# Performance work log

Measured on AMD Instinct MI355X. Metric: run time of the kernel, lower is better.

The kernel has to match this reference:

```python
import jax, jax.numpy as jnp
import numpy as np


def _ste(q, x):
    # straight-through estimator: forward = q, gradient = identity w.r.t. x
    return x + jax.lax.stop_gradient(q - x)


def quant_w(w, bit_w=8):
    # symmetric per-tensor weight quantization fused into QConv2d
    qmax = 2.0 ** (bit_w - 1) - 1.0
    scale = jnp.max(jnp.abs(w)) / qmax
    q = jnp.clip(jnp.round(w / scale), -qmax, qmax) * scale
    return _ste(q, w)


def quant_a(x, bit_a=8):
    # unsigned activation quantizer: clamp to [0,1], uniform bit_a levels
    n = 2.0 ** bit_a - 1.0
    xc = jnp.clip(x, 0.0, 1.0)
    q = jnp.round(xc * n) / n
    return _ste(q, xc)


def exp_norm2d(x, gamma, beta, eps=1e-5):
    # instance-style norm: per (N, C) statistics over spatial dims, affine
    mean = jnp.mean(x, axis=(2, 3), keepdims=True)
    var = jnp.var(x, axis=(2, 3), keepdims=True)
    xn = (x - mean) * jax.lax.rsqrt(var + eps)
    return xn * gamma[None, :, None, None] + beta[None, :, None, None]


def qconv(x, w, stride, pad, bit_w=8):
    wq = quant_w(w, bit_w)
    return jax.lax.conv_general_dilated(
        x, wq, window_strides=(stride, stride),
        padding=[(pad, pad), (pad, pad)],
        dimension_numbers=('NCHW', 'OIHW', 'NCHW'))


def setup_inputs() -> dict:
    key = jax.random.key(0)
    ks = jax.random.split(key, 4)
    C_in, C_out, H = 256, 512, 56
    return {
        'x': jax.random.normal(ks[0], (32, C_in, H, H), jnp.float32),
        'w1': jax.random.normal(ks[1], (C_out, C_in, 3, 3), jnp.float32) * 0.05,
        'g1': jnp.ones((C_out,), jnp.float32),
        'b1': jnp.zeros((C_out,), jnp.float32),
        'w2': jax.random.normal(ks[2], (C_out, C_out, 3, 3), jnp.float32) * 0.05,
        'g2': jnp.ones((C_out,), jnp.float32),
        'b2': jnp.zeros((C_out,), jnp.float32),
        'wp': jax.random.normal(ks[3], (C_out, C_in, 1, 1), jnp.float32) * 0.05,
        'gp': jnp.ones((C_out,), jnp.float32),
        'bp': jnp.zeros((C_out,), jnp.float32),
    }


def reference(x, w1, g1, b1, w2, g2, b2, wp, gp, bp):
    # main branch: QConv(s2) -> ExpNorm -> act quant -> QConv(s1) -> ExpNorm
    h = qconv(x, w1, stride=2, pad=1)
    h = exp_norm2d(h, g1, b1)
    h = quant_a(h, bit_a=8)
    h = qconv(h, w2, stride=1, pad=1)
    h = exp_norm2d(h, g2, b2)
    # projection shortcut: QConv 1x1 stride 2 -> ExpNorm
    s = qconv(x, wp, stride=2, pad=0)
    s = exp_norm2d(s, gp, bp)
    return h + s
```

## Files before the change

kernel.cpp:

```cpp
#include <hip/hip_runtime.h>
#include <cstdint>
#include <cstddef>


typedef unsigned short ushort_t;
typedef __attribute__((ext_vector_type(8))) short bf16x8;
typedef __attribute__((ext_vector_type(4))) float f32x4;
typedef __attribute__((ext_vector_type(4))) int i32x4;

#define NB   32
#define C_IN 256
#define HIN  56
#define CO   512
#define OHW  784
#define OWD  28
#define MTOT (NB * OHW)

constexpr size_t OFF_XH   = 0;
constexpr size_t OFF_A1   = OFF_XH  + 51380224;
constexpr size_t OFF_H2   = OFF_A1  + 25690112;
constexpr size_t OFF_S    = OFF_H2  + 51380224;
constexpr size_t OFF_WT1  = OFF_S   + 51380224;
constexpr size_t OFF_WT2  = OFF_WT1 + 2359296;
constexpr size_t OFF_WTP  = OFF_WT2 + 4718592;
constexpr size_t OFF_PSUM = OFF_WTP + 262144;
constexpr size_t OFF_A1N  = OFF_PSUM + 2097152;
constexpr size_t OFF_B1N  = OFF_A1N + 65536;
constexpr size_t OFF_A2N  = OFF_B1N + 65536;
constexpr size_t OFF_B2N  = OFF_A2N + 65536;
constexpr size_t OFF_APN  = OFF_B2N + 65536;
constexpr size_t OFF_BPN  = OFF_APN + 65536;
constexpr size_t OFF_MX   = OFF_BPN + 65536;
constexpr size_t OFF_ZB   = OFF_MX  + 16;
constexpr size_t OFF_CS   = OFF_ZB  + 2048;

__device__ __forceinline__ ushort_t f2bf(float f) {
    unsigned u = __float_as_uint(f);
    u += 0x7FFFu + ((u >> 16) & 1u);
    return (ushort_t)(u >> 16);
}
__device__ __forceinline__ float bf2f(ushort_t u) {
    return __uint_as_float(((unsigned)u) << 16);
}

__device__ __forceinline__ void async_copy16(const void* g, const void* l) {
    auto gp = (const __attribute__((address_space(1))) unsigned int*)(uintptr_t)g;
    auto lp = (__attribute__((address_space(3))) unsigned int*)(unsigned int)(uintptr_t)l;
    __builtin_amdgcn_global_load_lds(gp, lp, 16, 0, 0);
}

__global__ void to_nhwc_k(const float* __restrict__ x, ushort_t* __restrict__ xh) {
    __shared__ float tile[64][33];
    const int wt0 = blockIdx.x * 32;
    const int ct0 = blockIdx.y * 64;
    const int nh  = blockIdx.z;
    const int n = nh / HIN, h = nh - n * HIN;
    {
        const int tx = threadIdx.x & 31;
        const int ty = threadIdx.x >> 5;
        const int w  = wt0 + tx;
#pragma unroll
        for (int j = 0; j < 8; ++j) {
            int cl = ty + j * 8;
            if (w < HIN)
                tile[cl][tx] = x[(((size_t)n * C_IN + ct0 + cl) * HIN + h) * HIN + w];
        }
    }
    __syncthreads();
    {
        const int tc = threadIdx.x & 63;
        const int tw = threadIdx.x >> 6;
#pragma unroll
        for (int j = 0; j < 8; ++j) {
            int wl = tw + j * 4;
            int w  = wt0 + wl;
            if (w < HIN)
                xh[(((size_t)n * HIN + h) * HIN + w) * C_IN + ct0 + tc] =
                    f2bf(tile[tc][wl]);
        }
    }
}

__global__ void absmax3_k(const float* __restrict__ w1, int n1,
                          const float* __restrict__ w2, int n2,
                          const float* __restrict__ wp, int np,
                          unsigned* out) {
    const float* w; int nelem;
    if (blockIdx.y == 0)      { w = w1; nelem = n1; }
    else if (blockIdx.y == 1) { w = w2; nelem = n2; }
    else                      { w = wp; nelem = np; }
    int stride = gridDim.x * blockDim.x;
    float m = 0.f;
    for (int i = blockIdx.x * blockDim.x + threadIdx.x; i < nelem; i += stride)
        m = fmaxf(m, fabsf(w[i]));
#pragma unroll
    for (int off = 32; off > 0; off >>= 1)
        m = fmaxf(m, __shfl_down(m, off));
    if ((threadIdx.x & 63) == 0) atomicMax(out + blockIdx.y, __float_as_uint(m));
}

template <int CO_, int CI_, int KHW_>
__global__ void quantw_k(const float* __restrict__ w, const unsigned* __restrict__ mx,
                         ushort_t* __restrict__ wt) {
    const int total = KHW_ * CO_ * CI_;
    int idx = blockIdx.x * 256 + threadIdx.x;
    if (idx >= total) return;
    float scale = __uint_as_float(*mx) * (1.0f / 127.0f);
    float inv   = scale > 0.f ? 1.0f / scale : 0.f;
    int khw = idx / (CO_ * CI_);
    int r   = idx - khw * (CO_ * CI_);
    int co  = r / CI_;
    int ci  = r - co * CI_;
    float v  = w[((size_t)co * CI_ + ci) * KHW_ + khw];
    float qv = rintf(v * inv);
    qv = fminf(127.f, fmaxf(-127.f, qv));
    wt[idx] = f2bf(qv * scale);
}

__global__ void quantw_i8_k(const float* __restrict__ w, const unsigned* __restrict__ mx,
                            signed char* __restrict__ wt) {
    const int total = 9 * CO * CO;
    int idx = blockIdx.x * 256 + threadIdx.x;
    if (idx >= total) return;
    float scale = __uint_as_float(*mx) * (1.0f / 127.0f);
    float inv   = scale > 0.f ? 1.0f / scale : 0.f;
    int khw = idx / (CO * CO);
    int r   = idx - khw * (CO * CO);
    int co  = r / CO;
    int ci  = r - co * CO;
    float v  = w[((size_t)co * CO + ci) * 9 + khw];
    float qv = rintf(v * inv);
    qv = fminf(127.f, fmaxf(-127.f, qv));
    wt[idx] = (signed char)(int)qv;
}

__global__ void colsum_k(const signed char* __restrict__ wt, float* __restrict__ cs) {
    const int khw = blockIdx.x;
    const int co  = blockIdx.y * 32 + (threadIdx.x & 31);
    const int cig = threadIdx.x >> 5;
    const signed char* p = wt + ((size_t)khw * CO + co) * CO + cig * 64;
    int s = 0;
#pragma unroll
    for (int i = 0; i < 64; ++i) s += p[i];
    __shared__ int red[8][32];
    red[cig][threadIdx.x & 31] = s;
    __syncthreads();
    if (cig == 0) {
        int tot = 0;
#pragma unroll
        for (int g = 0; g < 8; ++g) tot += red[g][threadIdx.x & 31];
        cs[khw * CO + co] = (float)tot;
    }
}

template <int CIN, int KH, int KW, int STRIDE, int PAD, int IH, int IW>
__launch_bounds__(512, 2)
__global__ void conv8p_k(const ushort_t* __restrict__ xin,
                         const ushort_t* __restrict__ wt,
                         ushort_t* __restrict__ out,
                         const ushort_t* __restrict__ zbuf,
                         float* __restrict__ psum, float* __restrict__ pss) {
    constexpr int BK  = 64;
    constexpr int CKT = CIN / BK;
    constexpr int KT  = KH * KW * CKT;

    __shared__ alignas(16) short As[2 * 256 * BK];
    __shared__ alignas(16) short Bs[2 * 256 * BK];

    const int tid  = threadIdx.x;
    const int lane = tid & 63;
    const int wv   = tid >> 6;
    const int wm   = wv >> 2;
    const int wn   = wv & 3;
    const int lrow = lane & 15;
    const int lq   = lane >> 4;
    const int sw   = lrow & 7;

    const int bid = blockIdx.x;
    const int xcd = bid & 7;
    const int j   = bid >> 3;
    const int wg  = (xcd < 4 ? xcd * 25 : 100 + (xcd - 4) * 24) + j;
    const int m0  = (wg >> 1) * 256;
    const int co0 = (wg & 1) * 256;

    const int arow = tid >> 3;
    const int ach  = tid & 7;
    long abase[4]; unsigned amask[4]; int bco[4];
#pragma unroll
    for (int c = 0; c < 4; ++c) {
        int row = c * 64 + arow;
        int m   = m0 + row;
        int n   = m / OHW;
        int sp  = m - n * OHW;
        int oh  = sp / OWD, ow = sp - oh * OWD;
        int ihb = oh * STRIDE - PAD, iwb = ow * STRIDE - PAD;
        int swz = (ach ^ (row & 7)) * 8;
        abase[c] = ((long)n * (IH * IW) + (long)ihb * IW + iwb) * CIN + swz;
        unsigned mk = 0;
#pragma unroll
        for (int kh = 0; kh < KH; ++kh)
#pragma unroll
            for (int kw = 0; kw < KW; ++kw) {
                int ih = ihb + kh, iw = iwb + kw;
                if ((unsigned)ih < (unsigned)IH && (unsigned)iw < (unsigned)IW)
                    mk |= 1u << (kh * KW + kw);
            }
        amask[c] = mk;
        bco[c]   = (co0 + row) * CIN + swz;
    }

    auto stageA = [&](int c, int nb, long aoff, int khw) {
        const ushort_t* src = ((amask[c] >> khw) & 1)
            ? xin + (abase[c] + aoff) : zbuf;
        async_copy16(src, (const void*)&As[nb * 16384 + c * 4096 + wv * 512]);
    };
    auto stageB = [&](int c, int nb, int boff) {
        async_copy16(wt + (boff + bco[c]),
                     (const void*)&Bs[nb * 16384 + c * 4096 + wv * 512]);
    };

    f32x4 acc[8][4];
#pragma unroll
    for (int a = 0; a < 8; ++a)
#pragma unroll
        for (int b = 0; b < 4; ++b) acc[a][b] = {0.f, 0.f, 0.f, 0.f};

    stageB(0, 0, 0); stageB(1, 0, 0); stageB(2, 0, 0); stageB(3, 0, 0);
    stageA(0, 0, 0, 0); stageA(1, 0, 0, 0); stageA(2, 0, 0, 0); stageA(3, 0, 0, 0);
    asm volatile("s_waitcnt vmcnt(0)" ::: "memory");
    __builtin_amdgcn_s_barrier();

    int  khw_n = 0, kw_n = 0, ck_n = 1;
    long aoff_n = BK;
    int  boff_n = BK;

    int cur = 0;
    for (int t = 0; t < KT; ++t) {
        const bool hn = (t + 1 < KT);
        const int  nb = cur ^ 1;
        const short* Acur = &As[cur * 16384];
        const short* Bcur = &Bs[cur * 16384];

        if (hn) {
            stageB(0, nb, boff_n); stageB(1, nb, boff_n);
            stageB(2, nb, boff_n); stageB(3, nb, boff_n);
            stageA(0, nb, aoff_n, khw_n); stageA(1, nb, aoff_n, khw_n);
            stageA(2, nb, aoff_n, khw_n); stageA(3, nb, aoff_n, khw_n);
        }
        __builtin_amdgcn_sched_barrier(0);

        bf16x8 af[4][2], bfr[2][2][2];

#pragma unroll
        for (int mi = 0; mi < 4; ++mi) {
            const int row = wm * 128 + mi * 16 + lrow;
#pragma unroll
            for (int ks = 0; ks < 2; ++ks) {
                const int ch = ((ks * 4 + lq) ^ sw) * 8;
                af[mi][ks] = *(const bf16x8*)&Acur[row * BK + ch];
            }
        }
#pragma unroll
        for (int qn = 0; qn < 2; ++qn)
#pragma unroll
            for (int ni = 0; ni < 2; ++ni) {
                const int row = wn * 64 + qn * 32 + ni * 16 + lrow;
#pragma unroll
                for (int ks = 0; ks < 2; ++ks) {
                    const int ch = ((ks * 4 + lq) ^ sw) * 8;
                    bfr[qn][ni][ks] = *(const bf16x8*)&Bcur[row * BK + ch];
                }
            }
#pragma unroll
        for (int mi = 0; mi < 4; ++mi)
#pragma unroll
            for (int qn = 0; qn < 2; ++qn)
#pragma unroll
                for (int ni = 0; ni < 2; ++ni)
#pragma unroll
                    for (int ks = 0; ks < 2; ++ks)
                        acc[mi][qn * 2 + ni] =
                            __builtin_amdgcn_mfma_f32_16x16x32_bf16(
                                af[mi][ks], bfr[qn][ni][ks],
                                acc[mi][qn * 2 + ni], 0, 0, 0);

#pragma unroll
        for (int mi = 0; mi < 4; ++mi) {
            const int row = wm * 128 + 64 + mi * 16 + lrow;
#pragma unroll
            for (int ks = 0; ks < 2; ++ks) {
                const int ch = ((ks * 4 + lq) ^ sw) * 8;
                af[mi][ks] = *(const bf16x8*)&Acur[row * BK + ch];
            }
        }
#pragma unroll
        for (int mi = 0; mi < 4; ++mi)
#pragma unroll
            for (int qn = 0; qn < 2; ++qn)
#pragma unroll
                for (int ni = 0; ni < 2; ++ni)
#pragma unroll
                    for (int ks = 0; ks < 2; ++ks)
                        acc[4 + mi][qn * 2 + ni] =
                            __builtin_amdgcn_mfma_f32_16x16x32_bf16(
                                af[mi][ks], bfr[qn][ni][ks],
                                acc[4 + mi][qn * 2 + ni], 0, 0, 0);

        asm volatile("s_waitcnt vmcnt(0)" ::: "memory");
        __builtin_amdgcn_sched_barrier(0);
        __builtin_amdgcn_s_barrier();

        if (hn) {
            ck_n++;
            if (ck_n == CKT) {
                ck_n = 0; khw_n++; kw_n++;
                if (kw_n == KW) { kw_n = 0; aoff_n += (long)(IW - KW) * CIN + BK; }
                else            { aoff_n += BK; }
                boff_n += (CO - 1) * CIN + BK;
            } else {
                aoff_n += BK; boff_n += BK;
            }
        }
        cur ^= 1;
    }

    const int mb = m0 + wm * 128 + lq * 4;
    const int cb = co0 + wn * 64 + lrow;
#pragma unroll
    for (int mi = 0; mi < 8; ++mi)
#pragma unroll
        for (int ni = 0; ni < 4; ++ni)
#pragma unroll
            for (int r = 0; r < 4; ++r)
                out[(size_t)(mb + mi * 16 + r) * CO + (cb + ni * 16)] =
                    f2bf(acc[mi][ni][r]);

    const int n0 = m0 / OHW;
    const int mS = (n0 + 1) * OHW;
    float sv[2][4], qv[2][4];
#pragma unroll
    for (int g = 0; g < 2; ++g)
#pragma unroll
        for (int ni = 0; ni < 4; ++ni) { sv[g][ni] = 0.f; qv[g][ni] = 0.f; }
#pragma unroll
    for (int mi = 0; mi < 8; ++mi)
#pragma unroll
        for (int ni = 0; ni < 4; ++ni)
#pragma unroll
            for (int r = 0; r < 4; ++r) {
                float v = acc[mi][ni][r];
                int m = mb + mi * 16 + r;
                int g = (m >= mS) ? 1 : 0;
                sv[g][ni] += v; qv[g][ni] += v * v;
            }
#pragma unroll
    for (int d = 16; d <= 32; d <<= 1)
#pragma unroll
        for (int g = 0; g < 2; ++g)
#pragma unroll
            for (int ni = 0; ni < 4; ++ni) {
                sv[g][ni] += __shfl_xor(sv[g][ni], d);
                qv[g][ni] += __shfl_xor(qv[g][ni], d);
            }
    if (lq == 0) {
        const bool split = (mS < m0 + 256);
#pragma unroll
        for (int ni = 0; ni < 4; ++ni) {
            atomicAdd(&psum[n0 * CO + cb + ni * 16], sv[0][ni]);
            atomicAdd(&pss [n0 * CO + cb + ni * 16], qv[0][ni]);
            if (split) {
                atomicAdd(&psum[(n0 + 1) * CO + cb + ni * 16], sv[1][ni]);
                atomicAdd(&pss [(n0 + 1) * CO + cb + ni * 16], qv[1][ni]);
            }
        }
    }
}

__launch_bounds__(512, 2)
__global__ void conv_i8_k(const signed char* __restrict__ xin,
                          const signed char* __restrict__ wt,
                          const float* __restrict__ colsum,
                          const unsigned* __restrict__ mxp,
                          ushort_t* __restrict__ out,
                          const signed char* __restrict__ zbuf,
                          float* __restrict__ psum, float* __restrict__ pss) {
    constexpr int CIN = 512, BK = 64, CKT = 8, KT = 72;
    constexpr int IH = 28, IW = 28;

    __shared__ alignas(16) signed char As[2 * 256 * BK];
    __shared__ alignas(16) signed char Bs[2 * 256 * BK];

    const int tid  = threadIdx.x;
    const int lane = tid & 63;
    const int wv   = tid >> 6;
    const int wm   = wv >> 2;
    const int wn   = wv & 3;
    const int lrow = lane & 15;
    const int lq   = lane >> 4;

    const int bid = blockIdx.x;
    const int xcd = bid & 7;
    const int j   = bid >> 3;
    const int wg  = (xcd < 4 ? xcd * 25 : 100 + (xcd - 4) * 24) + j;
    const int m0  = (wg >> 1) * 256;
    const int co0 = (wg & 1) * 256;

    const int arow2 = tid >> 2;
    const int ach2  = tid & 3;
    long abase[2]; unsigned amask[2]; int bco[2];
#pragma unroll
    for (int c = 0; c < 2; ++c) {
        int row = c * 128 + arow2;
        int m   = m0 + row;
        int n   = m / OHW;
        int sp  = m - n * OHW;
        int oh  = sp / OWD, ow = sp - oh * OWD;
        int ihb = oh - 1, iwb = ow - 1;
        int swz = (ach2 ^ (row & 3)) * 16;
        abase[c] = ((long)n * (IH * IW) + (long)ihb * IW + iwb) * CIN + swz;
        unsigned mk = 0;
#pragma unroll
        for (int kh = 0; kh < 3; ++kh)
#pragma unroll
            for (int kw = 0; kw < 3; ++kw) {
                int ih = ihb + kh, iw = iwb + kw;
                if ((unsigned)ih < (unsigned)IH && (unsigned)iw < (unsigned)IW)
                    mk |= 1u << (kh * 3 + kw);
            }
        amask[c] = mk;
        bco[c]   = (co0 + row) * CIN + swz;
    }

    auto stageA = [&](int c, int nb, long aoff, int khw) {
        const signed char* src = ((amask[c] >> khw) & 1)
            ? xin + (abase[c] + aoff) : zbuf;
        async_copy16(src, (const void*)&As[nb * 16384 + c * 8192 + wv * 1024]);
    };
    auto stageB = [&](int c, int nb, int boff) {
        async_copy16(wt + (boff + bco[c]),
                     (const void*)&Bs[nb * 16384 + c * 8192 + wv * 1024]);
    };

    i32x4 acc[8][4];
#pragma unroll
    for (int a = 0; a < 8; ++a)
#pragma unroll
        for (int b = 0; b < 4; ++b) acc[a][b] = {0, 0, 0, 0};

    stageB(0, 0, 0); stageB(1, 0, 0);
    stageA(0, 0, 0, 0); stageA(1, 0, 0, 0);
    asm volatile("s_waitcnt vmcnt(0)" ::: "memory");
    __builtin_amdgcn_s_barrier();

    int  khw_n = 0, kw_n = 0, ck_n = 1;
    long aoff_n = BK;
    int  boff_n = BK;

    int cur = 0;
    for (int t = 0; t < KT; ++t) {
        const bool hn = (t + 1 < KT);
        const int  nb = cur ^ 1;
        const signed char* Acur = &As[cur * 16384];
        const signed char* Bcur = &Bs[cur * 16384];

        if (hn) {
            stageB(0, nb, boff_n); stageB(1, nb, boff_n);
            stageA(0, nb, aoff_n, khw_n); stageA(1, nb, aoff_n, khw_n);
        }
        __builtin_amdgcn_sched_barrier(0);

        i32x4 af[8], bfr[4];
#pragma unroll
        for (int mi = 0; mi < 8; ++mi) {
            const int row = wm * 128 + mi * 16 + lrow;
            const int byt = row * BK + ((lq ^ (row & 3)) * 16);
            af[mi] = *(const i32x4*)&Acur[byt];
        }
#pragma unroll
        for (int ni = 0; ni < 4; ++ni) {
            const int row = wn * 64 + ni * 16 + lrow;
            const int byt = row * BK + ((lq ^ (row & 3)) * 16);
            bfr[ni] = *(const i32x4*)&Bcur[byt];
        }
#pragma unroll
        for (int mi = 0; mi < 8; ++mi)
#pragma unroll
            for (int ni = 0; ni < 4; ++ni)
                acc[mi][ni] = __builtin_amdgcn_mfma_i32_16x16x64_i8(
                    af[mi], bfr[ni], acc[mi][ni], 0, 0, 0);

        asm volatile("s_waitcnt vmcnt(0)" ::: "memory");
        __builtin_amdgcn_sched_barrier(0);
        __builtin_amdgcn_s_barrier();

        if (hn) {
            ck_n++;
            if (ck_n == CKT) {
                ck_n = 0; khw_n++; kw_n++;
                if (kw_n == 3) { kw_n = 0; aoff_n += (long)(IW - 3) * CIN + BK; }
                else           { aoff_n += BK; }
                boff_n += (CO - 1) * CIN + BK;
            } else {
                aoff_n += BK; boff_n += BK;
            }
        }
        cur ^= 1;
    }

    const int mb = m0 + wm * 128 + lq * 4;
    const int cb = co0 + wn * 64 + lrow;
    const float scale = __uint_as_float(*mxp) * (1.0f / 127.0f);
    const float sc    = scale * (1.0f / 255.0f);
    const float c128  = 128.0f * sc;

    float Sall[4], Sr0[4], Sr2[4], Sc0[4], Sc2[4], K0[4], K2[4], K6[4], K8[4];
#pragma unroll
    for (int ni = 0; ni < 4; ++ni) {
        float cs[9];
#pragma unroll
        for (int k = 0; k < 9; ++k) cs[k] = colsum[k * CO + cb + ni * 16];
        Sall[ni] = cs[0]+cs[1]+cs[2]+cs[3]+cs[4]+cs[5]+cs[6]+cs[7]+cs[8];
        Sr0[ni] = cs[0]+cs[1]+cs[2];  Sr2[ni] = cs[6]+cs[7]+cs[8];
        Sc0[ni] = cs[0]+cs[3]+cs[6];  Sc2[ni] = cs[2]+cs[5]+cs[8];
        K0[ni] = cs[0]; K2[ni] = cs[2]; K6[ni] = cs[6]; K8[ni] = cs[8];
    }

    const int n0 = m0 / OHW;
    const int mS = (n0 + 1) * OHW;
    float sv[2][4], qvv[2][4];
#pragma unroll
    for (int g = 0; g < 2; ++g)
#pragma unroll
        for (int ni = 0; ni < 4; ++ni) { sv[g][ni] = 0.f; qvv[g][ni] = 0.f; }

#pragma unroll
    for (int mi = 0; mi < 8; ++mi)
#pragma unroll
        for (int r = 0; r < 4; ++r) {
            const int m  = mb + mi * 16 + r;
            const int n  = m / OHW;
            const int sp = m - n * OHW;
            const int oh = sp / OWD, ow = sp - oh * OWD;
            const int g  = (m >= mS) ? 1 : 0;
#pragma unroll
            for (int ni = 0; ni < 4; ++ni) {
                float T = Sall[ni];
                if (oh == 0)       T -= Sr0[ni];
                if (oh == OWD - 1) T -= Sr2[ni];
                if (ow == 0)       T -= Sc0[ni];
                if (ow == OWD - 1) T -= Sc2[ni];
                if (oh == 0 && ow == 0)             T += K0[ni];
                if (oh == 0 && ow == OWD - 1)       T += K2[ni];
                if (oh == OWD - 1 && ow == 0)       T += K6[ni];
                if (oh == OWD - 1 && ow == OWD - 1) T += K8[ni];
                float val = sc * (float)acc[mi][ni][r] + c128 * T;
                out[(size_t)m * CO + (cb + ni * 16)] = f2bf(val);
                sv[g][ni] += val; qvv[g][ni] += val * val;
            }
        }
#pragma unroll
    for (int d = 16; d <= 32; d <<= 1)
#pragma unroll
        for (int g = 0; g < 2; ++g)
#pragma unroll
            for (int ni = 0; ni < 4; ++ni) {
                sv[g][ni]  += __shfl_xor(sv[g][ni], d);
                qvv[g][ni] += __shfl_xor(qvv[g][ni], d);
            }
    if (lq == 0) {
        const bool split = (mS < m0 + 256);
#pragma unroll
        for (int ni = 0; ni < 4; ++ni) {
            atomicAdd(&psum[n0 * CO + cb + ni * 16], sv[0][ni]);
            atomicAdd(&pss [n0 * CO + cb + ni * 16], qvv[0][ni]);
            if (split) {
                atomicAdd(&psum[(n0 + 1) * CO + cb + ni * 16], sv[1][ni]);
                atomicAdd(&pss [(n0 + 1) * CO + cb + ni * 16], qvv[1][ni]);
            }
        }
    }
}

__global__ void statsf3_k(const float* __restrict__ ps0, const float* __restrict__ qs0,
                          const float* __restrict__ g0, const float* __restrict__ bb0,
                          float* __restrict__ ao0, float* __restrict__ bo0,
                          const float* __restrict__ ps1, const float* __restrict__ qs1,
                          const float* __restrict__ g1, const float* __restrict__ bb1,
                          float* __restrict__ ao1, float* __restrict__ bo1,
                          const float* __restrict__ ps2, const float* __restrict__ qs2,
                          const float* __restrict__ g2, const float* __restrict__ bb2,
                          float* __restrict__ ao2, float* __restrict__ bo2) {
    const float *ps, *qs, *g, *bb; float *ao, *bo;
    if (blockIdx.y == 0)      { ps = ps0; qs = qs0; g = g0; bb = bb0; ao = ao0; bo = bo0; }
    else if (blockIdx.y == 1) { ps = ps1; qs = qs1; g = g1; bb = bb1; ao = ao1; bo = bo1; }
    else                      { ps = ps2; qs = qs2; g = g2; bb = bb2; ao = ao2; bo = bo2; }
    int idx = blockIdx.x * 256 + threadIdx.x;
    int c = idx & 511;
    float s  = ps[idx];
    float ss = qs[idx];
    float mean = s * (1.0f / 784.0f);
    float var  = ss * (1.0f / 784.0f) - mean * mean;
    float rstd = rsqrtf(var + 1e-5f);
    float a = rstd * g[c];
    ao[idx] = a;
    bo[idx] = bb[c] - mean * a;
}

__global__ void norm_quant_i8_k(const ushort_t* __restrict__ h, const float* __restrict__ a_,
                                const float* __restrict__ b_, signed char* __restrict__ o) {
    int idx = blockIdx.x * 256 + threadIdx.x;
    int row = idx >> 6;
    int c0  = (idx & 63) * 8;
    int n   = row / OHW;
    bf16x8 v = ((const bf16x8*)h)[idx];
    const float* ap = a_ + n * CO + c0;
    const float* bp = b_ + n * CO + c0;
    unsigned lo = 0, hi = 0;
#pragma unroll
    for (int k = 0; k < 8; ++k) {
        float f = bf2f((ushort_t)v[k]) * ap[k] + bp[k];
        float kq = rintf(fminf(fmaxf(f, 0.f), 1.f) * 255.f);
        int s8 = (int)kq - 128;
        unsigned b = (unsigned)(s8 & 0xFF);
        if (k < 4) lo |= b << (8 * k);
        else       hi |= b << (8 * (k - 4));
    }
    ((uint2*)o)[idx] = make_uint2(lo, hi);
}

__global__ void final_k(const ushort_t* __restrict__ h2, const ushort_t* __restrict__ s,
                        const float* __restrict__ a2, const float* __restrict__ b2,
                        const float* __restrict__ ap_, const float* __restrict__ bp_,
                        float* __restrict__ out) {
    __shared__ float tile[64][33];
    const int sp0 = blockIdx.x * 32;
    const int c0  = blockIdx.y * 64;
    const int n   = blockIdx.z;
    const int tx  = threadIdx.x & 31;
    const int ty  = threadIdx.x >> 5;
#pragma unroll
    for (int j = 0; j < 4; ++j) {
        int spl = ty + j * 8;
        int sp  = sp0 + spl;
        if (sp < OHW) {
            int c = c0 + tx * 2;
            size_t ix = ((size_t)n * OHW + sp) * CO + c;
            int ci = n * CO + c;
            ushort2 vh = *(const ushort2*)&h2[ix];
            ushort2 vs = *(const ushort2*)&s[ix];
            tile[tx * 2][spl] =
                bf2f(vh.x) * a2[ci] + b2[ci] + bf2f(vs.x) * ap_[ci] + bp_[ci];
            tile[tx * 2 + 1][spl] =
                bf2f(vh.y) * a2[ci + 1] + b2[ci + 1] + bf2f(vs.y) * ap_[ci + 1] + bp_[ci + 1];
        }
    }
    __syncthreads();
    const int sp = sp0 + tx;
#pragma unroll
    for (int j = 0; j < 8; ++j) {
        int cl = ty + j * 8;
        if (sp < OHW)
            out[((size_t)n * CO + c0 + cl) * OHW + sp] = tile[cl][tx];
    }
}

extern "C" void kernel_launch(void* const* d_in, const int* in_sizes, int n_in,
                              void* d_out, int out_size, void* d_ws, size_t ws_size,
                              hipStream_t stream) {
    const float* x  = (const float*)d_in[0];
    const float* w1 = (const float*)d_in[1];
    const float* g1 = (const float*)d_in[2];
    const float* b1 = (const float*)d_in[3];
    const float* w2 = (const float*)d_in[4];
    const float* g2 = (const float*)d_in[5];
    const float* b2 = (const float*)d_in[6];
    const float* wp = (const float*)d_in[7];
    const float* gp = (const float*)d_in[8];
    const float* bp = (const float*)d_in[9];
    float* out = (float*)d_out;
    char* ws = (char*)d_ws;

    ushort_t*    xh    = (ushort_t*)(ws + OFF_XH);
    signed char* a1    = (signed char*)(ws + OFF_A1);
    ushort_t*    h2    = (ushort_t*)(ws + OFF_H2);
    ushort_t*    sbuf  = (ushort_t*)(ws + OFF_S);
    ushort_t*    wt1   = (ushort_t*)(ws + OFF_WT1);
    signed char* wt2i  = (signed char*)(ws + OFF_WT2);
    ushort_t*    wtp   = (ushort_t*)(ws + OFF_WTP);
    float*    psum1 = (float*)(ws + OFF_PSUM);
    float*    pss1  = (float*)(ws + OFF_PSUM + 65536);
    float*    psum2 = (float*)(ws + OFF_PSUM + 131072);
    float*    pss2  = (float*)(ws + OFF_PSUM + 196608);
    float*    psump = (float*)(ws + OFF_PSUM + 262144);
    float*    pssp  = (float*)(ws + OFF_PSUM + 327680);
    float*    a1n  = (float*)(ws + OFF_A1N);
    float*    b1n  = (float*)(ws + OFF_B1N);
    float*    a2n  = (float*)(ws + OFF_A2N);
    float*    b2n  = (float*)(ws + OFF_B2N);
    float*    apn  = (float*)(ws + OFF_APN);
    float*    bpn  = (float*)(ws + OFF_BPN);
    unsigned* mx   = (unsigned*)(ws + OFF_MX);
    ushort_t* zb   = (ushort_t*)(ws + OFF_ZB);
    float*    cs   = (float*)(ws + OFF_CS);
    ushort_t* h1   = (ushort_t*)out;

    hipMemsetAsync(ws + OFF_MX, 0, 16 + 2048, stream);
    hipMemsetAsync(ws + OFF_PSUM, 0, 393216, stream);

    to_nhwc_k<<<dim3(2, 4, NB * HIN), 256, 0, stream>>>(x, xh);
    absmax3_k<<<dim3(512, 3), 256, 0, stream>>>(w1, CO * C_IN * 9,
                                                w2, CO * CO * 9,
                                                wp, C_IN * CO, mx);
    quantw_k<CO, C_IN, 9><<<dim3(4608), 256, 0, stream>>>(w1, mx + 0, wt1);
    quantw_i8_k<<<dim3(9216), 256, 0, stream>>>(w2, mx + 1, wt2i);
    quantw_k<CO, C_IN, 1><<<dim3(512), 256, 0, stream>>>(wp, mx + 2, wtp);
    colsum_k<<<dim3(9, 16), 256, 0, stream>>>(wt2i, cs);

    conv8p_k<C_IN, 3, 3, 2, 1, HIN, HIN>
        <<<dim3(196), 512, 0, stream>>>(xh, wt1, h1, (const ushort_t*)zb, psum1, pss1);
    statsf3_k<<<dim3(64, 1), 256, 0, stream>>>(psum1, pss1, g1, b1, a1n, b1n,
                                               psum1, pss1, g1, b1, a1n, b1n,
                                               psum1, pss1, g1, b1, a1n, b1n);
    norm_quant_i8_k<<<dim3(MTOT * CO / 8 / 256), 256, 0, stream>>>(h1, a1n, b1n, a1);

    conv_i8_k<<<dim3(196), 512, 0, stream>>>(a1, wt2i, cs, mx + 1, h2,
                                             (const signed char*)zb, psum2, pss2);
    conv8p_k<C_IN, 1, 1, 2, 0, HIN, HIN>
        <<<dim3(196), 512, 0, stream>>>(xh, wtp, sbuf, (const ushort_t*)zb, psump, pssp);

    statsf3_k<<<dim3(64, 2), 256, 0, stream>>>(psum2, pss2, g2, b2, a2n, b2n,
                                               psump, pssp, gp, bp, apn, bpn,
                                               psum2, pss2, g2, b2, a2n, b2n);

    final_k<<<dim3(25, 8, NB), 256, 0, stream>>>(h2, sbuf, a2n, b2n, apn, bpn, out);
}
```

Before: 319.5 us.

## Shrink int8 conv tile to 128x128 and launch four times more blocks

Reworks the int8 3x3 conv from 256x256 output tiles over 196 blocks to 128x128 tiles over 784 blocks. LDS use drops to a quarter, launch bounds now allow 4 blocks per CU, the LDS swizzle pattern changes, the XCD-aware block remap is simplified and offsets move to 32-bit. The aim is better occupancy and more latency hiding on a GPU whose 196 blocks did not fill it. In exchange each tile gets less operand reuse, so more global and LDS traffic is needed per MFMA and there are more atomic stat updates.

```diff
diff --git a/kernel.cpp b/kernel.cpp
--- a/kernel.cpp
+++ b/kernel.cpp
@@ -376,7 +376,7 @@
     }
 }
 
-__launch_bounds__(512, 2)
+__launch_bounds__(512, 4)
 __global__ void conv_i8_k(const signed char* __restrict__ xin,
                           const signed char* __restrict__ wt,
                           const float* __restrict__ colsum,
@@ -387,8 +387,8 @@
     constexpr int CIN = 512, BK = 64, CKT = 8, KT = 72;
     constexpr int IH = 28, IW = 28;
 
-    __shared__ alignas(16) signed char As[2 * 256 * BK];
-    __shared__ alignas(16) signed char Bs[2 * 256 * BK];
+    __shared__ alignas(16) signed char As[2 * 128 * BK];
+    __shared__ alignas(16) signed char Bs[2 * 128 * BK];
 
     const int tid  = threadIdx.x;
     const int lane = tid & 63;
@@ -399,25 +399,22 @@
     const int lq   = lane >> 4;
 
     const int bid = blockIdx.x;
-    const int xcd = bid & 7;
-    const int j   = bid >> 3;
-    const int wg  = (xcd < 4 ? xcd * 25 : 100 + (xcd - 4) * 24) + j;
-    const int m0  = (wg >> 1) * 256;
-    const int co0 = (wg & 1) * 256;
-
-    const int arow2 = tid >> 2;
-    const int ach2  = tid & 3;
-    long abase[2]; unsigned amask[2]; int bco[2];
-#pragma unroll
-    for (int c = 0; c < 2; ++c) {
-        int row = c * 128 + arow2;
-        int m   = m0 + row;
+    const int wg  = (bid & 7) * 98 + (bid >> 3);
+    const int m0  = (wg >> 2) * 128;
+    const int co0 = (wg & 3) * 128;
+
+    const int arow = tid >> 2;
+    const int ach  = tid & 3;
+    const int fsw  = (arow >> 1) & 3;
+    int abase; unsigned amask; int bco;
+    {
+        int m   = m0 + arow;
         int n   = m / OHW;
         int sp  = m - n * OHW;
         int oh  = sp / OWD, ow = sp - oh * OWD;
         int ihb = oh - 1, iwb = ow - 1;
-        int swz = (ach2 ^ (row & 3)) * 16;
-        abase[c] = ((long)n * (IH * IW) + (long)ihb * IW + iwb) * CIN + swz;
+        int swz = (ach ^ fsw) * 16;
+        abase = (n * (IH * IW) + ihb * IW + iwb) * CIN + swz;
         unsigned mk = 0;
 #pragma unroll
         for (int kh = 0; kh < 3; ++kh)
@@ -427,65 +424,60 @@
                 if ((unsigned)ih < (unsigned)IH && (unsigned)iw < (unsigned)IW)
                     mk |= 1u << (kh * 3 + kw);
             }
-        amask[c] = mk;
-        bco[c]   = (co0 + row) * CIN + swz;
-    }
-
-    auto stageA = [&](int c, int nb, long aoff, int khw) {
-        const signed char* src = ((amask[c] >> khw) & 1)
-            ? xin + (abase[c] + aoff) : zbuf;
-        async_copy16(src, (const void*)&As[nb * 16384 + c * 8192 + wv * 1024]);
+        amask = mk;
+        bco = (co0 + arow) * CIN + swz;
+    }
+
+    auto stageA = [&](int nb, int aoff, int khw) {
+        const signed char* src = ((amask >> khw) & 1)
+            ? xin + (abase + aoff) : zbuf;
+        async_copy16(src, (const void*)&As[nb * 8192 + wv * 1024]);
     };
-    auto stageB = [&](int c, int nb, int boff) {
-        async_copy16(wt + (boff + bco[c]),
-                     (const void*)&Bs[nb * 16384 + c * 8192 + wv * 1024]);
+    auto stageB = [&](int nb, int boff) {
+        async_copy16(wt + (boff + bco),
+                     (const void*)&Bs[nb * 8192 + wv * 1024]);
     };
 
-    i32x4 acc[8][4];
-#pragma unroll
-    for (int a = 0; a < 8; ++a)
-#pragma unroll
-        for (int b = 0; b < 4; ++b) acc[a][b] = {0, 0, 0, 0};
-
-    stageB(0, 0, 0); stageB(1, 0, 0);
-    stageA(0, 0, 0, 0); stageA(1, 0, 0, 0);
+    i32x4 acc[4][2];
+#pragma unroll
+    for (int a = 0; a < 4; ++a)
+#pragma unroll
+        for (int b = 0; b < 2; ++b) acc[a][b] = {0, 0, 0, 0};
+
+    stageB(0, 0);
+    stageA(0, 0, 0);
     asm volatile("s_waitcnt vmcnt(0)" ::: "memory");
     __builtin_amdgcn_s_barrier();
 
-    int  khw_n = 0, kw_n = 0, ck_n = 1;
-    long aoff_n = BK;
-    int  boff_n = BK;
+    int khw_n = 0, kw_n = 0, ck_n = 1;
+    int aoff_n = BK;
+    int boff_n = BK;
 
     int cur = 0;
     for (int t = 0; t < KT; ++t) {
         const bool hn = (t + 1 < KT);
         const int  nb = cur ^ 1;
-        const signed char* Acur = &As[cur * 16384];
-        const signed char* Bcur = &Bs[cur * 16384];
-
-        if (hn) {
-            stageB(0, nb, boff_n); stageB(1, nb, boff_n);
-            stageA(0, nb, aoff_n, khw_n); stageA(1, nb, aoff_n, khw_n);
-        }
+        const signed char* Acur = &As[cur * 8192];
+        const signed char* Bcur = &Bs[cur * 8192];
+
+        if (hn) { stageB(nb, boff_n); stageA(nb, aoff_n, khw_n); }
         __builtin_amdgcn_sched_barrier(0);
 
-        i32x4 af[8], bfr[4];
-#pragma unroll
-        for (int mi = 0; mi < 8; ++mi) {
-            const int row = wm * 128 + mi * 16 + lrow;
-            const int byt = row * BK + ((lq ^ (row & 3)) * 16);
-            af[mi] = *(const i32x4*)&Acur[byt];
-        }
-#pragma unroll
-        for (int ni = 0; ni < 4; ++ni) {
-            const int row = wn * 64 + ni * 16 + lrow;
-            const int byt = row * BK + ((lq ^ (row & 3)) * 16);
-            bfr[ni] = *(const i32x4*)&Bcur[byt];
-        }
-#pragma unroll
-        for (int mi = 0; mi < 8; ++mi)
-#pragma unroll
-            for (int ni = 0; ni < 4; ++ni)
+        i32x4 af[4], bfr[2];
+#pragma unroll
+        for (int mi = 0; mi < 4; ++mi) {
+            const int row = wm * 64 + mi * 16 + lrow;
+            af[mi] = *(const i32x4*)&Acur[row * BK + ((lq ^ ((row >> 1) & 3)) * 16)];
+        }
+#pragma unroll
+        for (int ni = 0; ni < 2; ++ni) {
+            const int row = wn * 32 + ni * 16 + lrow;
+            bfr[ni] = *(const i32x4*)&Bcur[row * BK + ((lq ^ ((row >> 1) & 3)) * 16)];
+        }
+#pragma unroll
+        for (int mi = 0; mi < 4; ++mi)
+#pragma unroll
+            for (int ni = 0; ni < 2; ++ni)
                 acc[mi][ni] = __builtin_amdgcn_mfma_i32_16x16x64_i8(
                     af[mi], bfr[ni], acc[mi][ni], 0, 0, 0);
 
@@ -497,7 +489,7 @@
             ck_n++;
             if (ck_n == CKT) {
                 ck_n = 0; khw_n++; kw_n++;
-                if (kw_n == 3) { kw_n = 0; aoff_n += (long)(IW - 3) * CIN + BK; }
+                if (kw_n == 3) { kw_n = 0; aoff_n += (IW - 3) * CIN + BK; }
                 else           { aoff_n += BK; }
                 boff_n += (CO - 1) * CIN + BK;
             } else {
@@ -507,15 +499,15 @@
         cur ^= 1;
     }
 
-    const int mb = m0 + wm * 128 + lq * 4;
-    const int cb = co0 + wn * 64 + lrow;
+    const int mb = m0 + wm * 64 + lq * 4;
+    const int cb = co0 + wn * 32 + lrow;
     const float scale = __uint_as_float(*mxp) * (1.0f / 127.0f);
     const float sc    = scale * (1.0f / 255.0f);
     const float c128  = 128.0f * sc;
 
-    float Sall[4], Sr0[4], Sr2[4], Sc0[4], Sc2[4], K0[4], K2[4], K6[4], K8[4];
-#pragma unroll
-    for (int ni = 0; ni < 4; ++ni) {
+    float Sall[2], Sr0[2], Sr2[2], Sc0[2], Sc2[2], K0[2], K2[2], K6[2], K8[2];
+#pragma unroll
+    for (int ni = 0; ni < 2; ++ni) {
         float cs[9];
 #pragma unroll
         for (int k = 0; k < 9; ++k) cs[k] = colsum[k * CO + cb + ni * 16];
@@ -527,14 +519,14 @@
 
     const int n0 = m0 / OHW;
     const int mS = (n0 + 1) * OHW;
-    float sv[2][4], qvv[2][4];
+    float sv[2][2], qvv[2][2];
 #pragma unroll
     for (int g = 0; g < 2; ++g)
 #pragma unroll
-        for (int ni = 0; ni < 4; ++ni) { sv[g][ni] = 0.f; qvv[g][ni] = 0.f; }
-
-#pragma unroll
-    for (int mi = 0; mi < 8; ++mi)
+        for (int ni = 0; ni < 2; ++ni) { sv[g][ni] = 0.f; qvv[g][ni] = 0.f; }
+
+#pragma unroll
+    for (int mi = 0; mi < 4; ++mi)
 #pragma unroll
         for (int r = 0; r < 4; ++r) {
             const int m  = mb + mi * 16 + r;
@@ -543,7 +535,7 @@
             const int oh = sp / OWD, ow = sp - oh * OWD;
             const int g  = (m >= mS) ? 1 : 0;
 #pragma unroll
-            for (int ni = 0; ni < 4; ++ni) {
+            for (int ni = 0; ni < 2; ++ni) {
                 float T = Sall[ni];
                 if (oh == 0)       T -= Sr0[ni];
                 if (oh == OWD - 1) T -= Sr2[ni];
@@ -563,14 +555,14 @@
 #pragma unroll
         for (int g = 0; g < 2; ++g)
 #pragma unroll
-            for (int ni = 0; ni < 4; ++ni) {
+            for (int ni = 0; ni < 2; ++ni) {
                 sv[g][ni]  += __shfl_xor(sv[g][ni], d);
                 qvv[g][ni] += __shfl_xor(qvv[g][ni], d);
             }
     if (lq == 0) {
-        const bool split = (mS < m0 + 256);
-#pragma unroll
-        for (int ni = 0; ni < 4; ++ni) {
+        const bool split = (mS < m0 + 128);
+#pragma unroll
+        for (int ni = 0; ni < 2; ++ni) {
             atomicAdd(&psum[n0 * CO + cb + ni * 16], sv[0][ni]);
             atomicAdd(&pss [n0 * CO + cb + ni * 16], qvv[0][ni]);
             if (split) {
@@ -723,7 +715,7 @@
                                                psum1, pss1, g1, b1, a1n, b1n);
     norm_quant_i8_k<<<dim3(MTOT * CO / 8 / 256), 256, 0, stream>>>(h1, a1n, b1n, a1);
 
-    conv_i8_k<<<dim3(196), 512, 0, stream>>>(a1, wt2i, cs, mx + 1, h2,
+    conv_i8_k<<<dim3(784), 512, 0, stream>>>(a1, wt2i, cs, mx + 1, h2,
                                              (const signed char*)zb, psum2, pss2);
     conv8p_k<C_IN, 1, 1, 2, 0, HIN, HIN>
         <<<dim3(196), 512, 0, stream>>>(xh, wtp, sbuf, (const ushort_t*)zb, psump, pssp);
```

After: 342.5 us. 7.2% more time.

## Merge 3x3 and 1x1 strided convs into one launch; change int8 LDS swizzle

Applied to the files above, without the earlier changes.

The stride-2 3x3 conv and the 1x1 projection conv, both reading the NHWC input, now run as one kernel with 392 blocks. Each block picks its conv type from its block index, with the two types interleaved across XCDs. This is meant to fill the GPU with more concurrent work and let the cheap 1x1 tiles fill the tail of the 3x3 grid. In exchange the conv shape becomes runtime values, so loop unrolling and constant folding are lost. The int8 conv's LDS XOR swizzle also changes from row&3 to (row>>1)&3 to reduce bank conflicts.

```diff
diff --git a/kernel.cpp b/kernel.cpp
--- a/kernel.cpp
+++ b/kernel.cpp
@@ -153,16 +153,17 @@
     }
 }
 
-template <int CIN, int KH, int KW, int STRIDE, int PAD, int IH, int IW>
 __launch_bounds__(512, 2)
-__global__ void conv8p_k(const ushort_t* __restrict__ xin,
-                         const ushort_t* __restrict__ wt,
-                         ushort_t* __restrict__ out,
-                         const ushort_t* __restrict__ zbuf,
-                         float* __restrict__ psum, float* __restrict__ pss) {
-    constexpr int BK  = 64;
-    constexpr int CKT = CIN / BK;
-    constexpr int KT  = KH * KW * CKT;
+__global__ void convmix_k(const ushort_t* __restrict__ xin,
+                          const ushort_t* __restrict__ wt1,
+                          const ushort_t* __restrict__ wtp,
+                          ushort_t* __restrict__ out1,
+                          ushort_t* __restrict__ outp,
+                          const ushort_t* __restrict__ zbuf,
+                          float* __restrict__ psum1, float* __restrict__ pss1,
+                          float* __restrict__ psump, float* __restrict__ pssp) {
+    constexpr int CIN = 256, BK = 64, CKT = 4;
+    constexpr int IH = HIN, IW = HIN;
 
     __shared__ alignas(16) short As[2 * 256 * BK];
     __shared__ alignas(16) short Bs[2 * 256 * BK];
@@ -176,12 +177,21 @@
     const int lq   = lane >> 4;
     const int sw   = lrow & 7;
 
-    const int bid = blockIdx.x;
-    const int xcd = bid & 7;
-    const int j   = bid >> 3;
-    const int wg  = (xcd < 4 ? xcd * 25 : 100 + (xcd - 4) * 24) + j;
-    const int m0  = (wg >> 1) * 256;
-    const int co0 = (wg & 1) * 256;
+    const int bid  = blockIdx.x;
+    const int wg   = (bid & 7) * 49 + (bid >> 3);
+    const int type = wg & 1;
+    const int tl   = wg >> 1;
+    const int m0   = (tl >> 1) * 256;
+    const int co0  = (tl & 1) * 256;
+
+    const int KH  = type ? 1 : 3;
+    const int KW  = KH;
+    const int PAD = type ? 0 : 1;
+    const int KT  = KH * KW * CKT;
+    const ushort_t* wt  = type ? wtp : wt1;
+    ushort_t*       out = type ? outp : out1;
+    float* psum = type ? psump : psum1;
+    float* pss  = type ? pssp  : pss1;
 
     const int arow = tid >> 3;
     const int ach  = tid & 7;
@@ -193,13 +203,11 @@
         int n   = m / OHW;
         int sp  = m - n * OHW;
         int oh  = sp / OWD, ow = sp - oh * OWD;
-        int ihb = oh * STRIDE - PAD, iwb = ow * STRIDE - PAD;
+        int ihb = oh * 2 - PAD, iwb = ow * 2 - PAD;
         int swz = (ach ^ (row & 7)) * 8;
         abase[c] = ((long)n * (IH * IW) + (long)ihb * IW + iwb) * CIN + swz;
         unsigned mk = 0;
-#pragma unroll
         for (int kh = 0; kh < KH; ++kh)
-#pragma unroll
             for (int kw = 0; kw < KW; ++kw) {
                 int ih = ihb + kh, iw = iwb + kw;
                 if ((unsigned)ih < (unsigned)IH && (unsigned)iw < (unsigned)IW)
@@ -416,7 +424,7 @@
         int sp  = m - n * OHW;
         int oh  = sp / OWD, ow = sp - oh * OWD;
         int ihb = oh - 1, iwb = ow - 1;
-        int swz = (ach2 ^ (row & 3)) * 16;
+        int swz = (ach2 ^ ((row >> 1) & 3)) * 16;
         abase[c] = ((long)n * (IH * IW) + (long)ihb * IW + iwb) * CIN + swz;
         unsigned mk = 0;
 #pragma unroll
@@ -473,14 +481,12 @@
 #pragma unroll
         for (int mi = 0; mi < 8; ++mi) {
             const int row = wm * 128 + mi * 16 + lrow;
-            const int byt = row * BK + ((lq ^ (row & 3)) * 16);
-            af[mi] = *(const i32x4*)&Acur[byt];
+            af[mi] = *(const i32x4*)&Acur[row * BK + ((lq ^ ((row >> 1) & 3)) * 16)];
         }
 #pragma unroll
         for (int ni = 0; ni < 4; ++ni) {
             const int row = wn * 64 + ni * 16 + lrow;
-            const int byt = row * BK + ((lq ^ (row & 3)) * 16);
-            bfr[ni] = *(const i32x4*)&Bcur[byt];
+            bfr[ni] = *(const i32x4*)&Bcur[row * BK + ((lq ^ ((row >> 1) & 3)) * 16)];
         }
 #pragma unroll
         for (int mi = 0; mi < 8; ++mi)
@@ -716,8 +722,9 @@
     quantw_k<CO, C_IN, 1><<<dim3(512), 256, 0, stream>>>(wp, mx + 2, wtp);
     colsum_k<<<dim3(9, 16), 256, 0, stream>>>(wt2i, cs);
 
-    conv8p_k<C_IN, 3, 3, 2, 1, HIN, HIN>
-        <<<dim3(196), 512, 0, stream>>>(xh, wt1, h1, (const ushort_t*)zb, psum1, pss1);
+    convmix_k<<<dim3(392), 512, 0, stream>>>(xh, wt1, wtp, h1, sbuf,
+                                             (const ushort_t*)zb,
+                                             psum1, pss1, psump, pssp);
     statsf3_k<<<dim3(64, 1), 256, 0, stream>>>(psum1, pss1, g1, b1, a1n, b1n,
                                                psum1, pss1, g1, b1, a1n, b1n,
                                                psum1, pss1, g1, b1, a1n, b1n);
@@ -725,8 +732,6 @@
 
     conv_i8_k<<<dim3(196), 512, 0, stream>>>(a1, wt2i, cs, mx + 1, h2,
                                              (const signed char*)zb, psum2, pss2);
-    conv8p_k<C_IN, 1, 1, 2, 0, HIN, HIN>
-        <<<dim3(196), 512, 0, stream>>>(xh, wtp, sbuf, (const ushort_t*)zb, psump, pssp);
 
     statsf3_k<<<dim3(64, 2), 256, 0, stream>>>(psum2, pss2, g2, b2, a2n, b2n,
                                                psump, pssp, gp, bp, apn, bpn,
```

Measured after the change: 357.8 us. +12.0%, slower.
